# Kernel tuning notes

Measured on AMD Instinct MI355X. Metric: run time of the kernel, lower is better.

Reference implementation:

```python
import jax, jax.numpy as jnp
import numpy as np

N = 50000      # nodes
E = 800000     # edges
IN = 128       # in_channels
HID = 64       # hidden_channels per head
HEADS = 2
OUT = 64       # out_channels of second conv
ED = 16        # edge_dim
NEG = 0.2      # LeakyReLU negative slope (PyG default)


def setup_inputs() -> dict:
    key = jax.random.key(0)
    ks = jax.random.split(key, 24)
    def p(k, shape, scale=0.05):
        return jax.random.normal(k, shape, jnp.float32) * scale
    inp = {}
    inp["x"] = jax.random.normal(ks[0], (N, IN), jnp.float32)
    inp["edge_index"] = jax.random.randint(ks[1], (2, E), 0, N, jnp.int32)
    inp["edge_attr"] = jax.random.normal(ks[2], (E, ED), jnp.float32)
    # GATv2Conv layer 1 (heads=HEADS, out=HID)
    inp["Wl1"] = p(ks[3], (IN, HEADS * HID)); inp["bl1"] = jnp.zeros((HEADS * HID,), jnp.float32)
    inp["Wr1"] = p(ks[4], (IN, HEADS * HID)); inp["br1"] = jnp.zeros((HEADS * HID,), jnp.float32)
    inp["We1"] = p(ks[5], (ED, HEADS * HID))
    inp["att1"] = p(ks[6], (HEADS, HID))
    inp["b1"] = jnp.zeros((HEADS * HID,), jnp.float32)
    # GATv2Conv layer 2 (heads=1, out=OUT), input dim = HEADS*HID
    inp["Wl2"] = p(ks[7], (HEADS * HID, OUT)); inp["bl2"] = jnp.zeros((OUT,), jnp.float32)
    inp["Wr2"] = p(ks[8], (HEADS * HID, OUT)); inp["br2"] = jnp.zeros((OUT,), jnp.float32)
    inp["We2"] = p(ks[9], (ED, OUT))
    inp["att2"] = p(ks[10], (1, OUT))
    inp["b2"] = jnp.zeros((OUT,), jnp.float32)
    # edge MLP: Linear(2*OUT, OUT) -> ReLU -> Linear(OUT, 1)
    inp["Wm1"] = p(ks[11], (2 * OUT, OUT)); inp["bm1"] = jnp.zeros((OUT,), jnp.float32)
    inp["Wm2"] = p(ks[12], (OUT, 1)); inp["bm2"] = jnp.zeros((1,), jnp.float32)
    return inp


def add_self_loops(src, dst, edge_attr, n):
    # PyG add_self_loops with fill_value='mean': loop attr = mean of incoming edge attrs
    cnt = jax.ops.segment_sum(jnp.ones((src.shape[0],), edge_attr.dtype), dst, num_segments=n)
    loop_attr = jax.ops.segment_sum(edge_attr, dst, num_segments=n) / jnp.maximum(cnt, 1.0)[:, None]
    ar = jnp.arange(n, dtype=src.dtype)
    return (jnp.concatenate([src, ar]), jnp.concatenate([dst, ar]),
            jnp.concatenate([edge_attr, loop_attr], axis=0))


def gatv2_layer(x, src, dst, edge_attr, Wl, bl, Wr, br, We, att, bias, heads, out_ch):
    n = x.shape[0]
    xl = (x @ Wl + bl).reshape(n, heads, out_ch)   # messages (source side)
    xr = (x @ Wr + br).reshape(n, heads, out_ch)   # target side
    ea = (edge_attr @ We).reshape(-1, heads, out_ch)
    m = jax.nn.leaky_relu(xl[src] + xr[dst] + ea, NEG)      # [Et, H, C]
    logits = jnp.einsum('ehc,hc->eh', m, att)               # [Et, H]
    # segment softmax over destination node (every node has a self loop)
    mx = jax.ops.segment_max(logits, dst, num_segments=n)
    ex = jnp.exp(logits - mx[dst])
    den = jax.ops.segment_sum(ex, dst, num_segments=n)
    alpha = ex / den[dst]                                   # [Et, H]
    out = jax.ops.segment_sum(alpha[:, :, None] * xl[src], dst, num_segments=n)
    return out.reshape(n, heads * out_ch) + bias


def reference(x, edge_index, edge_attr,
              Wl1, bl1, Wr1, br1, We1, att1, b1,
              Wl2, bl2, Wr2, br2, We2, att2, b2,
              Wm1, bm1, Wm2, bm2):
    src, dst = edge_index[0], edge_index[1]
    n = x.shape[0]
    s2, d2, ea2 = add_self_loops(src, dst, edge_attr, n)
    h = gatv2_layer(x, s2, d2, ea2, Wl1, bl1, Wr1, br1, We1, att1, b1, HEADS, HID)
    h = jax.nn.elu(h)
    h = gatv2_layer(h, s2, d2, ea2, Wl2, bl2, Wr2, br2, We2, att2, b2, 1, OUT)
    # edge predictor over the ORIGINAL edges
    ei = jnp.concatenate([h[src], h[dst]], axis=1)          # [E, 2*OUT]
    z = jax.nn.relu(ei @ Wm1 + bm1)
    return z @ Wm2 + bm2                                    # [E, 1]
```

## Files before the change

kernel.cpp:

```cpp
#include <hip/hip_runtime.h>
#include <cstdint>
#include <cstddef>


__device__ __forceinline__ float half_sum(float v) {
#pragma unroll
  for (int o = 1; o <= 16; o <<= 1) v += __shfl_xor(v, o, 64);
  return v;
}

__global__ __launch_bounds__(256) void cnt_kernel(const int* __restrict__ dst,
                                                  int* __restrict__ cnt, int E) {
  int e = blockIdx.x * 256 + threadIdx.x;
  if (e < E) atomicAdd(&cnt[dst[e]], 1);
}

__global__ __launch_bounds__(1024) void scan_kernel(
    const int* __restrict__ cnt, int* __restrict__ rowptr,
    int* __restrict__ cursor, int Nn) {
  __shared__ int part[1024];
  int t = threadIdx.x;
  int chunk = (Nn + 1023) / 1024;
  int lo = t * chunk, hi = min(lo + chunk, Nn);
  int s = 0;
  for (int i = lo; i < hi; i++) s += cnt[i] + 1;
  part[t] = s;
  __syncthreads();
  for (int o = 1; o < 1024; o <<= 1) {
    int v = (t >= o) ? part[t - o] : 0;
    __syncthreads();
    part[t] += v;
    __syncthreads();
  }
  int run = (t == 0) ? 0 : part[t - 1];
  for (int i = lo; i < hi; i++) {
    rowptr[i] = run;
    cursor[i] = run;
    run += cnt[i] + 1;
  }
  if (t == 1023) rowptr[Nn] = part[1023];
}

__global__ __launch_bounds__(256) void csr_build_kernel(
    const int* __restrict__ src, const int* __restrict__ dst,
    int* __restrict__ cursor, int* __restrict__ eperm,
    int* __restrict__ sperm, int E, int Et) {
  int e = blockIdx.x * 256 + threadIdx.x;
  if (e >= Et) return;
  int s, d;
  if (e < E) { s = src[e]; d = dst[e]; }
  else { s = e - E; d = s; }
  int pos = atomicAdd(&cursor[d], 1);
  eperm[pos] = e;
  sperm[pos] = s;
}

__global__ __launch_bounds__(256) void loop_attr_kernel(
    const int* __restrict__ rowptr, const int* __restrict__ eperm,
    const float* __restrict__ edge_attr, float* __restrict__ loop_attr,
    int Nn, int E) {
  int wid = blockIdx.x * 4 + (threadIdx.x >> 6);
  if (wid >= Nn) return;
  int l = threadIdx.x & 63;
  int sub = l >> 4, kk = l & 15;
  int start = rowptr[wid], end = rowptr[wid + 1];
  float acc = 0.f;
  for (int j = start + sub; j < end; j += 4) {
    int e = eperm[j];
    if (e < E) acc += edge_attr[(size_t)e * 16 + kk];
  }
  acc += __shfl_xor(acc, 16, 64);
  acc += __shfl_xor(acc, 32, 64);
  if (sub == 0) {
    float c = fmaxf((float)(end - start - 1), 1.f);
    loop_attr[(size_t)wid * 16 + kk] = acc / c;
  }
}

template <int K, int NC>
__global__ __launch_bounds__(256) void gemm_kernel(
    const float* __restrict__ A, const float* __restrict__ W,
    const float* __restrict__ bias, float* __restrict__ C, int M) {
  const int BM = 64;
  const int CQ = NC / 4;
  const int RP = BM / (256 / CQ);
  __shared__ float Alds[BM * K];
  int row0 = blockIdx.x * BM;
  for (int i = threadIdx.x; i < BM * K / 4; i += 256) {
    int r = i / (K / 4);
    float4 v = make_float4(0.f, 0.f, 0.f, 0.f);
    if (row0 + r < M) v = ((const float4*)A)[(size_t)(row0 + r) * (K / 4) + (i % (K / 4))];
    ((float4*)Alds)[i] = v;
  }
  __syncthreads();
  int cq = threadIdx.x % CQ;
  int rg = threadIdx.x / CQ;
  float4 acc[RP];
#pragma unroll
  for (int r = 0; r < RP; r++) acc[r] = make_float4(0.f, 0.f, 0.f, 0.f);
  const float4* W4 = (const float4*)W;
  for (int k = 0; k < K; k += 4) {
    float4 w0 = W4[(size_t)(k + 0) * CQ + cq];
    float4 w1 = W4[(size_t)(k + 1) * CQ + cq];
    float4 w2 = W4[(size_t)(k + 2) * CQ + cq];
    float4 w3 = W4[(size_t)(k + 3) * CQ + cq];
#pragma unroll
    for (int r = 0; r < RP; r++) {
      float4 a = ((const float4*)Alds)[(rg * RP + r) * (K / 4) + (k >> 2)];
      acc[r].x = fmaf(a.x, w0.x, acc[r].x);
      acc[r].y = fmaf(a.x, w0.y, acc[r].y);
      acc[r].z = fmaf(a.x, w0.z, acc[r].z);
      acc[r].w = fmaf(a.x, w0.w, acc[r].w);
      acc[r].x = fmaf(a.y, w1.x, acc[r].x);
      acc[r].y = fmaf(a.y, w1.y, acc[r].y);
      acc[r].z = fmaf(a.y, w1.z, acc[r].z);
      acc[r].w = fmaf(a.y, w1.w, acc[r].w);
      acc[r].x = fmaf(a.z, w2.x, acc[r].x);
      acc[r].y = fmaf(a.z, w2.y, acc[r].y);
      acc[r].z = fmaf(a.z, w2.z, acc[r].z);
      acc[r].w = fmaf(a.z, w2.w, acc[r].w);
      acc[r].x = fmaf(a.w, w3.x, acc[r].x);
      acc[r].y = fmaf(a.w, w3.y, acc[r].y);
      acc[r].z = fmaf(a.w, w3.z, acc[r].z);
      acc[r].w = fmaf(a.w, w3.w, acc[r].w);
    }
  }
  float4 b4 = bias ? ((const float4*)bias)[cq] : make_float4(0.f, 0.f, 0.f, 0.f);
#pragma unroll
  for (int r = 0; r < RP; r++) {
    int row = row0 + rg * RP + r;
    if (row < M) {
      float4 o = make_float4(acc[r].x + b4.x, acc[r].y + b4.y,
                             acc[r].z + b4.z, acc[r].w + b4.w);
      ((float4*)C)[(size_t)row * CQ + cq] = o;
    }
  }
}

template <int ELU>
__global__ __launch_bounds__(256) void node_fused2_kernel(
    const int* __restrict__ rowptr, const int* __restrict__ eperm,
    const int* __restrict__ sperm, const float* __restrict__ edge_attr,
    const float* __restrict__ loop_attr, const float* __restrict__ We,
    const float* __restrict__ att, const float* __restrict__ xl,
    const float* __restrict__ xr, const float* __restrict__ bias,
    float* __restrict__ out, int Nn, int E) {
  int wid = blockIdx.x * 4 + (threadIdx.x >> 6);
  if (wid >= Nn) return;
  int l = threadIdx.x & 63;
  int ch = ((l >> 5) << 6) | ((l & 31) << 1);
  float2 we[16];
#pragma unroll
  for (int k = 0; k < 16; k++) we[k] = *(const float2*)(We + k * 128 + ch);
  float2 xr2 = *(const float2*)(xr + (size_t)wid * 128 + ch);
  float2 at2 = *(const float2*)(att + ch);
  int start = __builtin_amdgcn_readfirstlane(rowptr[wid]);
  int end = __builtin_amdgcn_readfirstlane(rowptr[wid + 1]);
  float4 A0, A1, A2, A3;
  float2 X;
  int e_n, s_n;
  {
    int e_c = eperm[start], s_c = sperm[start];
    const float4* p4 = (const float4*)((e_c < E)
                           ? edge_attr + (size_t)e_c * 16
                           : loop_attr + (size_t)(e_c - E) * 16);
    A0 = p4[0]; A1 = p4[1]; A2 = p4[2]; A3 = p4[3];
    X = *(const float2*)(xl + (size_t)s_c * 128 + ch);
    int j1 = min(start + 1, end - 1);
    e_n = eperm[j1];
    s_n = sperm[j1];
  }
  float m = -1e30f, sden = 0.f, accx = 0.f, accy = 0.f;
  for (int j = start; j < end; ++j) {
    int j2 = min(j + 2, end - 1);
    int e2 = eperm[j2], s2 = sperm[j2];
    const float4* p4 = (const float4*)((e_n < E)
                           ? edge_attr + (size_t)e_n * 16
                           : loop_attr + (size_t)(e_n - E) * 16);
    float4 B0 = p4[0], B1 = p4[1], B2 = p4[2], B3 = p4[3];
    float2 Y = *(const float2*)(xl + (size_t)s_n * 128 + ch);
    float av[16] = {A0.x, A0.y, A0.z, A0.w, A1.x, A1.y, A1.z, A1.w,
                    A2.x, A2.y, A2.z, A2.w, A3.x, A3.y, A3.z, A3.w};
    float ex = 0.f, ey = 0.f;
#pragma unroll
    for (int k = 0; k < 16; k++) {
      ex = fmaf(av[k], we[k].x, ex);
      ey = fmaf(av[k], we[k].y, ey);
    }
    float mx = X.x + xr2.x + ex;
    float my = X.y + xr2.y + ey;
    mx = (mx >= 0.f) ? mx : 0.2f * mx;
    my = (my >= 0.f) ? my : 0.2f * my;
    float p = half_sum(fmaf(at2.x, mx, at2.y * my));
    float nm = fmaxf(m, p);
    float r = __expf(m - nm), ep = __expf(p - nm);
    sden = fmaf(sden, r, ep);
    accx = fmaf(accx, r, ep * X.x);
    accy = fmaf(accy, r, ep * X.y);
    m = nm;
    A0 = B0; A1 = B1; A2 = B2; A3 = B3; X = Y;
    e_n = e2; s_n = s2;
  }
  float inv = 1.f / sden;
  float2 b2 = *(const float2*)(bias + ch);
  float vx = fmaf(accx, inv, b2.x);
  float vy = fmaf(accy, inv, b2.y);
  if (ELU) {
    vx = (vx > 0.f) ? vx : expm1f(vx);
    vy = (vy > 0.f) ? vy : expm1f(vy);
  }
  *(float2*)(out + (size_t)wid * 128 + ch) = make_float2(vx, vy);
}

__global__ __launch_bounds__(256) void node_fused1_kernel(
    const int* __restrict__ rowptr, const int* __restrict__ eperm,
    const int* __restrict__ sperm, const float* __restrict__ edge_attr,
    const float* __restrict__ loop_attr, const float* __restrict__ We,
    const float* __restrict__ att, const float* __restrict__ xl,
    const float* __restrict__ xr, const float* __restrict__ bias,
    float* __restrict__ out, int Nn, int E) {
  int wid = blockIdx.x * 4 + (threadIdx.x >> 6);
  if (wid >= Nn) return;
  int l = threadIdx.x & 63;
  int half = l >> 5;
  int ch = (l & 31) << 1;
  float2 we[16];
#pragma unroll
  for (int k = 0; k < 16; k++) we[k] = *(const float2*)(We + k * 64 + ch);
  float2 xr2 = *(const float2*)(xr + (size_t)wid * 64 + ch);
  float2 at2 = *(const float2*)(att + ch);
  int start = __builtin_amdgcn_readfirstlane(rowptr[wid]);
  int end = __builtin_amdgcn_readfirstlane(rowptr[wid + 1]);
  float4 A0, A1, A2, A3;
  float2 X;
  int e_n, s_n;
  {
    int jc = min(start + half, end - 1);
    int e_c = eperm[jc], s_c = sperm[jc];
    const float4* p4 = (const float4*)((e_c < E)
                           ? edge_attr + (size_t)e_c * 16
                           : loop_attr + (size_t)(e_c - E) * 16);
    A0 = p4[0]; A1 = p4[1]; A2 = p4[2]; A3 = p4[3];
    X = *(const float2*)(xl + (size_t)s_c * 64 + ch);
    int j1 = min(start + 2 + half, end - 1);
    e_n = eperm[j1];
    s_n = sperm[j1];
  }
  float m = -1e30f, sden = 0.f, accx = 0.f, accy = 0.f;
  for (int j = start; j < end; j += 2) {
    int j2 = min(j + 4 + half, end - 1);
    int e2 = eperm[j2], s2 = sperm[j2];
    const float4* p4 = (const float4*)((e_n < E)
                           ? edge_attr + (size_t)e_n * 16
                           : loop_attr + (size_t)(e_n - E) * 16);
    float4 B0 = p4[0], B1 = p4[1], B2 = p4[2], B3 = p4[3];
    float2 Y = *(const float2*)(xl + (size_t)s_n * 64 + ch);
    float av[16] = {A0.x, A0.y, A0.z, A0.w, A1.x, A1.y, A1.z, A1.w,
                    A2.x, A2.y, A2.z, A2.w, A3.x, A3.y, A3.z, A3.w};
    float ex = 0.f, ey = 0.f;
#pragma unroll
    for (int k = 0; k < 16; k++) {
      ex = fmaf(av[k], we[k].x, ex);
      ey = fmaf(av[k], we[k].y, ey);
    }
    float mx = X.x + xr2.x + ex;
    float my = X.y + xr2.y + ey;
    mx = (mx >= 0.f) ? mx : 0.2f * mx;
    my = (my >= 0.f) ? my : 0.2f * my;
    float p = half_sum(fmaf(at2.x, mx, at2.y * my));
    bool dead = (j + half) >= end;
    p = dead ? -1e30f : p;
    float nm = fmaxf(m, p);
    float r = __expf(m - nm), ep = __expf(p - nm);
    ep = dead ? 0.f : ep;
    sden = fmaf(sden, r, ep);
    accx = fmaf(accx, r, ep * X.x);
    accy = fmaf(accy, r, ep * X.y);
    m = nm;
    A0 = B0; A1 = B1; A2 = B2; A3 = B3; X = Y;
    e_n = e2; s_n = s2;
  }
  float mo = __shfl_xor(m, 32, 64);
  float so = __shfl_xor(sden, 32, 64);
  float aox = __shfl_xor(accx, 32, 64);
  float aoy = __shfl_xor(accy, 32, 64);
  float M = fmaxf(m, mo);
  float ra = __expf(m - M), rb = __expf(mo - M);
  float S = fmaf(sden, ra, so * rb);
  float AX = fmaf(accx, ra, aox * rb);
  float AY = fmaf(accy, ra, aoy * rb);
  float inv = 1.f / S;
  if (half == 0) {
    float2 b2 = *(const float2*)(bias + ch);
    *(float2*)(out + (size_t)wid * 64 + ch) =
        make_float2(fmaf(AX, inv, b2.x), fmaf(AY, inv, b2.y));
  }
}

__global__ __launch_bounds__(256) void edge_mlp_kernel(
    const int* __restrict__ src, const int* __restrict__ dst,
    const float* __restrict__ aa, const float* __restrict__ bb,
    const float* __restrict__ Wm2, const float* __restrict__ bm2,
    float* __restrict__ out, int E) {
  int t = blockIdx.x * 256 + threadIdx.x;
  int eid = t >> 4;
  if (eid >= E) return;
  int g = threadIdx.x & 15;
  float4 w = ((const float4*)Wm2)[g];
  int s = src[eid], d = dst[eid];
  float4 za = ((const float4*)aa)[(size_t)s * 16 + g];
  float4 zb = ((const float4*)bb)[(size_t)d * 16 + g];
  float p = fmaxf(za.x + zb.x, 0.f) * w.x;
  p = fmaf(fmaxf(za.y + zb.y, 0.f), w.y, p);
  p = fmaf(fmaxf(za.z + zb.z, 0.f), w.z, p);
  p = fmaf(fmaxf(za.w + zb.w, 0.f), w.w, p);
#pragma unroll
  for (int o = 8; o > 0; o >>= 1) p += __shfl_xor(p, o, 64);
  if (g == 0) out[eid] = p + bm2[0];
}

extern "C" void kernel_launch(void* const* d_in, const int* in_sizes, int n_in,
                              void* d_out, int out_size, void* d_ws,
                              size_t ws_size, hipStream_t stream) {
  const float* x = (const float*)d_in[0];
  const int* ei = (const int*)d_in[1];
  const float* edge_attr = (const float*)d_in[2];
  const float* Wl1 = (const float*)d_in[3];
  const float* bl1 = (const float*)d_in[4];
  const float* Wr1 = (const float*)d_in[5];
  const float* br1 = (const float*)d_in[6];
  const float* We1 = (const float*)d_in[7];
  const float* att1 = (const float*)d_in[8];
  const float* b1 = (const float*)d_in[9];
  const float* Wl2 = (const float*)d_in[10];
  const float* bl2 = (const float*)d_in[11];
  const float* Wr2 = (const float*)d_in[12];
  const float* br2 = (const float*)d_in[13];
  const float* We2 = (const float*)d_in[14];
  const float* att2 = (const float*)d_in[15];
  const float* b2 = (const float*)d_in[16];
  const float* Wm1 = (const float*)d_in[17];
  const float* bm1 = (const float*)d_in[18];
  const float* Wm2 = (const float*)d_in[19];
  const float* bm2 = (const float*)d_in[20];

  const int Nn = in_sizes[0] / 128;
  const int E = in_sizes[1] / 2;
  const int Et = E + Nn;
  const int* src = ei;
  const int* dst = ei + E;

  char* ws = (char*)d_ws;
  size_t off = 0;
  auto alloc = [&](size_t bytes) -> char* {
    char* p = ws + off;
    off += (bytes + 255) & ~(size_t)255;
    return p;
  };
  int* cnt = (int*)alloc((size_t)Nn * 4);
  float* loop_attr = (float*)alloc((size_t)Nn * 16 * 4);
  int* rowptr = (int*)alloc((size_t)(Nn + 1) * 4);
  int* cursor = (int*)alloc((size_t)Nn * 4);
  int* eperm = (int*)alloc((size_t)Et * 4);
  int* sperm = (int*)alloc((size_t)Et * 4);
  float* xl = (float*)alloc((size_t)Nn * 128 * 4);
  float* xr = (float*)alloc((size_t)Nn * 128 * 4);
  float* h1 = (float*)alloc((size_t)Nn * 128 * 4);
  float* h2 = (float*)alloc((size_t)Nn * 64 * 4);
  float* aa = xl;
  float* bb = xr;

  hipMemsetAsync(cnt, 0, (size_t)Nn * 4, stream);

  cnt_kernel<<<(E + 255) / 256, 256, 0, stream>>>(dst, cnt, E);
  scan_kernel<<<1, 1024, 0, stream>>>(cnt, rowptr, cursor, Nn);
  csr_build_kernel<<<(Et + 255) / 256, 256, 0, stream>>>(src, dst, cursor, eperm,
                                                         sperm, E, Et);
  loop_attr_kernel<<<(Nn + 3) / 4, 256, 0, stream>>>(rowptr, eperm, edge_attr,
                                                     loop_attr, Nn, E);

  gemm_kernel<128, 128><<<(Nn + 63) / 64, 256, 0, stream>>>(x, Wl1, bl1, xl, Nn);
  gemm_kernel<128, 128><<<(Nn + 63) / 64, 256, 0, stream>>>(x, Wr1, br1, xr, Nn);
  node_fused2_kernel<1><<<(Nn + 3) / 4, 256, 0, stream>>>(
      rowptr, eperm, sperm, edge_attr, loop_attr, We1, att1, xl, xr, b1, h1, Nn, E);

  gemm_kernel<128, 64><<<(Nn + 63) / 64, 256, 0, stream>>>(h1, Wl2, bl2, xl, Nn);
  gemm_kernel<128, 64><<<(Nn + 63) / 64, 256, 0, stream>>>(h1, Wr2, br2, xr, Nn);
  node_fused1_kernel<<<(Nn + 3) / 4, 256, 0, stream>>>(
      rowptr, eperm, sperm, edge_attr, loop_attr, We2, att2, xl, xr, b2, h2, Nn, E);

  gemm_kernel<64, 64><<<(Nn + 63) / 64, 256, 0, stream>>>(h2, Wm1, nullptr, aa, Nn);
  gemm_kernel<64, 64><<<(Nn + 63) / 64, 256, 0, stream>>>(h2, Wm1 + 64 * 64, bm1,
                                                          bb, Nn);
  edge_mlp_kernel<<<(E * 16 + 255) / 256, 256, 0, stream>>>(src, dst, aa, bb,
                                                            Wm2, bm2,
                                                            (float*)d_out, E);
}
```

Before: 798.0 us.

## Fold self-loop edges into node kernels, fuse paired GEMMs, parallelize CSR scan

Self-loops are no longer stored in the CSR. Each node kernel handles its own loop edge at the end, taking the loop edge projection as the mean of the incoming edge projections accumulated in the loop. By linearity this equals projecting the mean attribute, so the separate loop_attr kernel and the per-edge branch go away. The eperm/sperm arrays are merged into one int2 array, and the single-block serial scan is replaced by a three-kernel parallel scan. Paired GEMMs sharing an input are fused into one kernel that reads A once and writes two outputs, at the cost of higher register pressure under a launch-bounds occupancy hint.

```diff
diff --git a/kernel.cpp b/kernel.cpp
--- a/kernel.cpp
+++ b/kernel.cpp
@@ -15,72 +15,73 @@
   if (e < E) atomicAdd(&cnt[dst[e]], 1);
 }
 
-__global__ __launch_bounds__(1024) void scan_kernel(
-    const int* __restrict__ cnt, int* __restrict__ rowptr,
-    int* __restrict__ cursor, int Nn) {
-  __shared__ int part[1024];
+__global__ __launch_bounds__(256) void scan_blocksum_kernel(
+    const int* __restrict__ cnt, int* __restrict__ partial, int Nn) {
+  int i = blockIdx.x * 256 + threadIdx.x;
+  int v = (i < Nn) ? cnt[i] : 0;
+#pragma unroll
+  for (int o = 32; o > 0; o >>= 1) v += __shfl_xor(v, o, 64);
+  __shared__ int ws[4];
+  if ((threadIdx.x & 63) == 0) ws[threadIdx.x >> 6] = v;
+  __syncthreads();
+  if (threadIdx.x == 0) partial[blockIdx.x] = ws[0] + ws[1] + ws[2] + ws[3];
+}
+
+__global__ __launch_bounds__(256) void scan_partial_kernel(
+    int* __restrict__ partial, int* __restrict__ rowptr, int nb, int Nn, int E) {
+  __shared__ int buf[256];
   int t = threadIdx.x;
-  int chunk = (Nn + 1023) / 1024;
-  int lo = t * chunk, hi = min(lo + chunk, Nn);
-  int s = 0;
-  for (int i = lo; i < hi; i++) s += cnt[i] + 1;
-  part[t] = s;
+  int v = (t < nb) ? partial[t] : 0;
+  buf[t] = v;
   __syncthreads();
-  for (int o = 1; o < 1024; o <<= 1) {
-    int v = (t >= o) ? part[t - o] : 0;
+  for (int o = 1; o < 256; o <<= 1) {
+    int u = (t >= o) ? buf[t - o] : 0;
     __syncthreads();
-    part[t] += v;
+    buf[t] += u;
     __syncthreads();
   }
-  int run = (t == 0) ? 0 : part[t - 1];
-  for (int i = lo; i < hi; i++) {
-    rowptr[i] = run;
-    cursor[i] = run;
-    run += cnt[i] + 1;
-  }
-  if (t == 1023) rowptr[Nn] = part[1023];
+  partial[t] = (t == 0) ? 0 : buf[t - 1];
+  if (t == 0) rowptr[Nn] = E;
+}
+
+__global__ __launch_bounds__(256) void scan_write_kernel(
+    const int* __restrict__ cnt, const int* __restrict__ partial,
+    int* __restrict__ rowptr, int* __restrict__ cursor, int Nn) {
+  __shared__ int buf[256];
+  int i = blockIdx.x * 256 + threadIdx.x;
+  int t = threadIdx.x;
+  int v = (i < Nn) ? cnt[i] : 0;
+  buf[t] = v;
+  __syncthreads();
+  for (int o = 1; o < 256; o <<= 1) {
+    int u = (t >= o) ? buf[t - o] : 0;
+    __syncthreads();
+    buf[t] += u;
+    __syncthreads();
+  }
+  if (i < Nn) {
+    int r = partial[blockIdx.x] + buf[t] - v;
+    rowptr[i] = r;
+    cursor[i] = r;
+  }
 }
 
 __global__ __launch_bounds__(256) void csr_build_kernel(
     const int* __restrict__ src, const int* __restrict__ dst,
-    int* __restrict__ cursor, int* __restrict__ eperm,
-    int* __restrict__ sperm, int E, int Et) {
+    int* __restrict__ cursor, int2* __restrict__ es, int E) {
   int e = blockIdx.x * 256 + threadIdx.x;
-  if (e >= Et) return;
-  int s, d;
-  if (e < E) { s = src[e]; d = dst[e]; }
-  else { s = e - E; d = s; }
+  if (e >= E) return;
+  int s = src[e], d = dst[e];
   int pos = atomicAdd(&cursor[d], 1);
-  eperm[pos] = e;
-  sperm[pos] = s;
-}
-
-__global__ __launch_bounds__(256) void loop_attr_kernel(
-    const int* __restrict__ rowptr, const int* __restrict__ eperm,
-    const float* __restrict__ edge_attr, float* __restrict__ loop_attr,
-    int Nn, int E) {
-  int wid = blockIdx.x * 4 + (threadIdx.x >> 6);
-  if (wid >= Nn) return;
-  int l = threadIdx.x & 63;
-  int sub = l >> 4, kk = l & 15;
-  int start = rowptr[wid], end = rowptr[wid + 1];
-  float acc = 0.f;
-  for (int j = start + sub; j < end; j += 4) {
-    int e = eperm[j];
-    if (e < E) acc += edge_attr[(size_t)e * 16 + kk];
-  }
-  acc += __shfl_xor(acc, 16, 64);
-  acc += __shfl_xor(acc, 32, 64);
-  if (sub == 0) {
-    float c = fmaxf((float)(end - start - 1), 1.f);
-    loop_attr[(size_t)wid * 16 + kk] = acc / c;
-  }
+  es[pos] = make_int2(e, s);
 }
 
 template <int K, int NC>
-__global__ __launch_bounds__(256) void gemm_kernel(
-    const float* __restrict__ A, const float* __restrict__ W,
-    const float* __restrict__ bias, float* __restrict__ C, int M) {
+__global__ __launch_bounds__(256, 4) void gemm2_kernel(
+    const float* __restrict__ A, const float* __restrict__ W1,
+    const float* __restrict__ b1, float* __restrict__ C1,
+    const float* __restrict__ W2, const float* __restrict__ b2,
+    float* __restrict__ C2, int M) {
   const int BM = 64;
   const int CQ = NC / 4;
   const int RP = BM / (256 / CQ);
@@ -95,56 +96,83 @@
   __syncthreads();
   int cq = threadIdx.x % CQ;
   int rg = threadIdx.x / CQ;
-  float4 acc[RP];
-#pragma unroll
-  for (int r = 0; r < RP; r++) acc[r] = make_float4(0.f, 0.f, 0.f, 0.f);
-  const float4* W4 = (const float4*)W;
+  float4 acc1[RP], acc2[RP];
+#pragma unroll
+  for (int r = 0; r < RP; r++) {
+    acc1[r] = make_float4(0.f, 0.f, 0.f, 0.f);
+    acc2[r] = make_float4(0.f, 0.f, 0.f, 0.f);
+  }
+  const float4* W14 = (const float4*)W1;
+  const float4* W24 = (const float4*)W2;
   for (int k = 0; k < K; k += 4) {
-    float4 w0 = W4[(size_t)(k + 0) * CQ + cq];
-    float4 w1 = W4[(size_t)(k + 1) * CQ + cq];
-    float4 w2 = W4[(size_t)(k + 2) * CQ + cq];
-    float4 w3 = W4[(size_t)(k + 3) * CQ + cq];
+    float4 u0 = W14[(size_t)(k + 0) * CQ + cq];
+    float4 u1 = W14[(size_t)(k + 1) * CQ + cq];
+    float4 u2 = W14[(size_t)(k + 2) * CQ + cq];
+    float4 u3 = W14[(size_t)(k + 3) * CQ + cq];
+    float4 v0 = W24[(size_t)(k + 0) * CQ + cq];
+    float4 v1 = W24[(size_t)(k + 1) * CQ + cq];
+    float4 v2 = W24[(size_t)(k + 2) * CQ + cq];
+    float4 v3 = W24[(size_t)(k + 3) * CQ + cq];
 #pragma unroll
     for (int r = 0; r < RP; r++) {
       float4 a = ((const float4*)Alds)[(rg * RP + r) * (K / 4) + (k >> 2)];
-      acc[r].x = fmaf(a.x, w0.x, acc[r].x);
-      acc[r].y = fmaf(a.x, w0.y, acc[r].y);
-      acc[r].z = fmaf(a.x, w0.z, acc[r].z);
-      acc[r].w = fmaf(a.x, w0.w, acc[r].w);
-      acc[r].x = fmaf(a.y, w1.x, acc[r].x);
-      acc[r].y = fmaf(a.y, w1.y, acc[r].y);
-      acc[r].z = fmaf(a.y, w1.z, acc[r].z);
-      acc[r].w = fmaf(a.y, w1.w, acc[r].w);
-      acc[r].x = fmaf(a.z, w2.x, acc[r].x);
-      acc[r].y = fmaf(a.z, w2.y, acc[r].y);
-      acc[r].z = fmaf(a.z, w2.z, acc[r].z);
-      acc[r].w = fmaf(a.z, w2.w, acc[r].w);
-      acc[r].x = fmaf(a.w, w3.x, acc[r].x);
-      acc[r].y = fmaf(a.w, w3.y, acc[r].y);
-      acc[r].z = fmaf(a.w, w3.z, acc[r].z);
-      acc[r].w = fmaf(a.w, w3.w, acc[r].w);
-    }
-  }
-  float4 b4 = bias ? ((const float4*)bias)[cq] : make_float4(0.f, 0.f, 0.f, 0.f);
+      acc1[r].x = fmaf(a.x, u0.x, acc1[r].x);
+      acc1[r].y = fmaf(a.x, u0.y, acc1[r].y);
+      acc1[r].z = fmaf(a.x, u0.z, acc1[r].z);
+      acc1[r].w = fmaf(a.x, u0.w, acc1[r].w);
+      acc1[r].x = fmaf(a.y, u1.x, acc1[r].x);
+      acc1[r].y = fmaf(a.y, u1.y, acc1[r].y);
+      acc1[r].z = fmaf(a.y, u1.z, acc1[r].z);
+      acc1[r].w = fmaf(a.y, u1.w, acc1[r].w);
+      acc1[r].x = fmaf(a.z, u2.x, acc1[r].x);
+      acc1[r].y = fmaf(a.z, u2.y, acc1[r].y);
+      acc1[r].z = fmaf(a.z, u2.z, acc1[r].z);
+      acc1[r].w = fmaf(a.z, u2.w, acc1[r].w);
+      acc1[r].x = fmaf(a.w, u3.x, acc1[r].x);
+      acc1[r].y = fmaf(a.w, u3.y, acc1[r].y);
+      acc1[r].z = fmaf(a.w, u3.z, acc1[r].z);
+      acc1[r].w = fmaf(a.w, u3.w, acc1[r].w);
+      acc2[r].x = fmaf(a.x, v0.x, acc2[r].x);
+      acc2[r].y = fmaf(a.x, v0.y, acc2[r].y);
+      acc2[r].z = fmaf(a.x, v0.z, acc2[r].z);
+      acc2[r].w = fmaf(a.x, v0.w, acc2[r].w);
+      acc2[r].x = fmaf(a.y, v1.x, acc2[r].x);
+      acc2[r].y = fmaf(a.y, v1.y, acc2[r].y);
+      acc2[r].z = fmaf(a.y, v1.z, acc2[r].z);
+      acc2[r].w = fmaf(a.y, v1.w, acc2[r].w);
+      acc2[r].x = fmaf(a.z, v2.x, acc2[r].x);
+      acc2[r].y = fmaf(a.z, v2.y, acc2[r].y);
+      acc2[r].z = fmaf(a.z, v2.z, acc2[r].z);
+      acc2[r].w = fmaf(a.z, v2.w, acc2[r].w);
+      acc2[r].x = fmaf(a.w, v3.x, acc2[r].x);
+      acc2[r].y = fmaf(a.w, v3.y, acc2[r].y);
+      acc2[r].z = fmaf(a.w, v3.z, acc2[r].z);
+      acc2[r].w = fmaf(a.w, v3.w, acc2[r].w);
+    }
+  }
+  float4 bb1 = b1 ? ((const float4*)b1)[cq] : make_float4(0.f, 0.f, 0.f, 0.f);
+  float4 bb2 = b2 ? ((const float4*)b2)[cq] : make_float4(0.f, 0.f, 0.f, 0.f);
 #pragma unroll
   for (int r = 0; r < RP; r++) {
     int row = row0 + rg * RP + r;
     if (row < M) {
-      float4 o = make_float4(acc[r].x + b4.x, acc[r].y + b4.y,
-                             acc[r].z + b4.z, acc[r].w + b4.w);
-      ((float4*)C)[(size_t)row * CQ + cq] = o;
+      ((float4*)C1)[(size_t)row * CQ + cq] =
+          make_float4(acc1[r].x + bb1.x, acc1[r].y + bb1.y, acc1[r].z + bb1.z,
+                      acc1[r].w + bb1.w);
+      ((float4*)C2)[(size_t)row * CQ + cq] =
+          make_float4(acc2[r].x + bb2.x, acc2[r].y + bb2.y, acc2[r].z + bb2.z,
+                      acc2[r].w + bb2.w);
     }
   }
 }
 
 template <int ELU>
-__global__ __launch_bounds__(256) void node_fused2_kernel(
-    const int* __restrict__ rowptr, const int* __restrict__ eperm,
-    const int* __restrict__ sperm, const float* __restrict__ edge_attr,
-    const float* __restrict__ loop_attr, const float* __restrict__ We,
+__global__ __launch_bounds__(256, 4) void node_fused2_kernel(
+    const int* __restrict__ rowptr, const int2* __restrict__ es,
+    const float* __restrict__ edge_attr, const float* __restrict__ We,
     const float* __restrict__ att, const float* __restrict__ xl,
     const float* __restrict__ xr, const float* __restrict__ bias,
-    float* __restrict__ out, int Nn, int E) {
+    float* __restrict__ out, int Nn) {
   int wid = blockIdx.x * 4 + (threadIdx.x >> 6);
   if (wid >= Nn) return;
   int l = threadIdx.x & 63;
@@ -156,50 +184,62 @@
   float2 at2 = *(const float2*)(att + ch);
   int start = __builtin_amdgcn_readfirstlane(rowptr[wid]);
   int end = __builtin_amdgcn_readfirstlane(rowptr[wid + 1]);
-  float4 A0, A1, A2, A3;
-  float2 X;
-  int e_n, s_n;
+  float m = -1e30f, sden = 0.f, accx = 0.f, accy = 0.f;
+  float sax = 0.f, say = 0.f;
+  if (end > start) {
+    float4 A0, A1, A2, A3;
+    float2 X;
+    int2 en;
+    {
+      int2 ec = es[start];
+      const float4* p4 = (const float4*)(edge_attr + (size_t)ec.x * 16);
+      A0 = p4[0]; A1 = p4[1]; A2 = p4[2]; A3 = p4[3];
+      X = *(const float2*)(xl + (size_t)ec.y * 128 + ch);
+      en = es[min(start + 1, end - 1)];
+    }
+    for (int j = start; j < end; ++j) {
+      int2 e2 = es[min(j + 2, end - 1)];
+      const float4* p4 = (const float4*)(edge_attr + (size_t)en.x * 16);
+      float4 B0 = p4[0], B1 = p4[1], B2 = p4[2], B3 = p4[3];
+      float2 Y = *(const float2*)(xl + (size_t)en.y * 128 + ch);
+      float av[16] = {A0.x, A0.y, A0.z, A0.w, A1.x, A1.y, A1.z, A1.w,
+                      A2.x, A2.y, A2.z, A2.w, A3.x, A3.y, A3.z, A3.w};
+      float ex = 0.f, ey = 0.f;
+#pragma unroll
+      for (int k = 0; k < 16; k++) {
+        ex = fmaf(av[k], we[k].x, ex);
+        ey = fmaf(av[k], we[k].y, ey);
+      }
+      sax += ex;
+      say += ey;
+      float mx = X.x + xr2.x + ex;
+      float my = X.y + xr2.y + ey;
+      mx = (mx >= 0.f) ? mx : 0.2f * mx;
+      my = (my >= 0.f) ? my : 0.2f * my;
+      float p = half_sum(fmaf(at2.x, mx, at2.y * my));
+      float nm = fmaxf(m, p);
+      float r = __expf(m - nm), ep = __expf(p - nm);
+      sden = fmaf(sden, r, ep);
+      accx = fmaf(accx, r, ep * X.x);
+      accy = fmaf(accy, r, ep * X.y);
+      m = nm;
+      A0 = B0; A1 = B1; A2 = B2; A3 = B3; X = Y;
+      en = e2;
+    }
+  }
   {
-    int e_c = eperm[start], s_c = sperm[start];
-    const float4* p4 = (const float4*)((e_c < E)
-                           ? edge_attr + (size_t)e_c * 16
-                           : loop_attr + (size_t)(e_c - E) * 16);
-    A0 = p4[0]; A1 = p4[1]; A2 = p4[2]; A3 = p4[3];
-    X = *(const float2*)(xl + (size_t)s_c * 128 + ch);
-    int j1 = min(start + 1, end - 1);
-    e_n = eperm[j1];
-    s_n = sperm[j1];
-  }
-  float m = -1e30f, sden = 0.f, accx = 0.f, accy = 0.f;
-  for (int j = start; j < end; ++j) {
-    int j2 = min(j + 2, end - 1);
-    int e2 = eperm[j2], s2 = sperm[j2];
-    const float4* p4 = (const float4*)((e_n < E)
-                           ? edge_attr + (size_t)e_n * 16
-                           : loop_attr + (size_t)(e_n - E) * 16);
-    float4 B0 = p4[0], B1 = p4[1], B2 = p4[2], B3 = p4[3];
-    float2 Y = *(const float2*)(xl + (size_t)s_n * 128 + ch);
-    float av[16] = {A0.x, A0.y, A0.z, A0.w, A1.x, A1.y, A1.z, A1.w,
-                    A2.x, A2.y, A2.z, A2.w, A3.x, A3.y, A3.z, A3.w};
-    float ex = 0.f, ey = 0.f;
-#pragma unroll
-    for (int k = 0; k < 16; k++) {
-      ex = fmaf(av[k], we[k].x, ex);
-      ey = fmaf(av[k], we[k].y, ey);
-    }
-    float mx = X.x + xr2.x + ex;
-    float my = X.y + xr2.y + ey;
+    float denom = 1.f / fmaxf((float)(end - start), 1.f);
+    float2 Xs = *(const float2*)(xl + (size_t)wid * 128 + ch);
+    float mx = Xs.x + xr2.x + sax * denom;
+    float my = Xs.y + xr2.y + say * denom;
     mx = (mx >= 0.f) ? mx : 0.2f * mx;
     my = (my >= 0.f) ? my : 0.2f * my;
     float p = half_sum(fmaf(at2.x, mx, at2.y * my));
     float nm = fmaxf(m, p);
     float r = __expf(m - nm), ep = __expf(p - nm);
     sden = fmaf(sden, r, ep);
-    accx = fmaf(accx, r, ep * X.x);
-    accy = fmaf(accy, r, ep * X.y);
-    m = nm;
-    A0 = B0; A1 = B1; A2 = B2; A3 = B3; X = Y;
-    e_n = e2; s_n = s2;
+    accx = fmaf(accx, r, ep * Xs.x);
+    accy = fmaf(accy, r, ep * Xs.y);
   }
   float inv = 1.f / sden;
   float2 b2 = *(const float2*)(bias + ch);
@@ -212,13 +252,12 @@
   *(float2*)(out + (size_t)wid * 128 + ch) = make_float2(vx, vy);
 }
 
-__global__ __launch_bounds__(256) void node_fused1_kernel(
-    const int* __restrict__ rowptr, const int* __restrict__ eperm,
-    const int* __restrict__ sperm, const float* __restrict__ edge_attr,
-    const float* __restrict__ loop_attr, const float* __restrict__ We,
+__global__ __launch_bounds__(256, 4) void node_fused1_kernel(
+    const int* __restrict__ rowptr, const int2* __restrict__ es,
+    const float* __restrict__ edge_attr, const float* __restrict__ We,
     const float* __restrict__ att, const float* __restrict__ xl,
     const float* __restrict__ xr, const float* __restrict__ bias,
-    float* __restrict__ out, int Nn, int E) {
+    float* __restrict__ out, int Nn) {
   int wid = blockIdx.x * 4 + (threadIdx.x >> 6);
   if (wid >= Nn) return;
   int l = threadIdx.x & 63;
@@ -231,54 +270,52 @@
   float2 at2 = *(const float2*)(att + ch);
   int start = __builtin_amdgcn_readfirstlane(rowptr[wid]);
   int end = __builtin_amdgcn_readfirstlane(rowptr[wid + 1]);
-  float4 A0, A1, A2, A3;
-  float2 X;
-  int e_n, s_n;
-  {
-    int jc = min(start + half, end - 1);
-    int e_c = eperm[jc], s_c = sperm[jc];
-    const float4* p4 = (const float4*)((e_c < E)
-                           ? edge_attr + (size_t)e_c * 16
-                           : loop_attr + (size_t)(e_c - E) * 16);
-    A0 = p4[0]; A1 = p4[1]; A2 = p4[2]; A3 = p4[3];
-    X = *(const float2*)(xl + (size_t)s_c * 64 + ch);
-    int j1 = min(start + 2 + half, end - 1);
-    e_n = eperm[j1];
-    s_n = sperm[j1];
-  }
   float m = -1e30f, sden = 0.f, accx = 0.f, accy = 0.f;
-  for (int j = start; j < end; j += 2) {
-    int j2 = min(j + 4 + half, end - 1);
-    int e2 = eperm[j2], s2 = sperm[j2];
-    const float4* p4 = (const float4*)((e_n < E)
-                           ? edge_attr + (size_t)e_n * 16
-                           : loop_attr + (size_t)(e_n - E) * 16);
-    float4 B0 = p4[0], B1 = p4[1], B2 = p4[2], B3 = p4[3];
-    float2 Y = *(const float2*)(xl + (size_t)s_n * 64 + ch);
-    float av[16] = {A0.x, A0.y, A0.z, A0.w, A1.x, A1.y, A1.z, A1.w,
-                    A2.x, A2.y, A2.z, A2.w, A3.x, A3.y, A3.z, A3.w};
-    float ex = 0.f, ey = 0.f;
-#pragma unroll
-    for (int k = 0; k < 16; k++) {
-      ex = fmaf(av[k], we[k].x, ex);
-      ey = fmaf(av[k], we[k].y, ey);
-    }
-    float mx = X.x + xr2.x + ex;
-    float my = X.y + xr2.y + ey;
-    mx = (mx >= 0.f) ? mx : 0.2f * mx;
-    my = (my >= 0.f) ? my : 0.2f * my;
-    float p = half_sum(fmaf(at2.x, mx, at2.y * my));
-    bool dead = (j + half) >= end;
-    p = dead ? -1e30f : p;
-    float nm = fmaxf(m, p);
-    float r = __expf(m - nm), ep = __expf(p - nm);
-    ep = dead ? 0.f : ep;
-    sden = fmaf(sden, r, ep);
-    accx = fmaf(accx, r, ep * X.x);
-    accy = fmaf(accy, r, ep * X.y);
-    m = nm;
-    A0 = B0; A1 = B1; A2 = B2; A3 = B3; X = Y;
-    e_n = e2; s_n = s2;
+  float sax = 0.f, say = 0.f;
+  if (end > start) {
+    float4 A0, A1, A2, A3;
+    float2 X;
+    int2 en;
+    {
+      int jc = min(start + half, end - 1);
+      int2 ec = es[jc];
+      const float4* p4 = (const float4*)(edge_attr + (size_t)ec.x * 16);
+      A0 = p4[0]; A1 = p4[1]; A2 = p4[2]; A3 = p4[3];
+      X = *(const float2*)(xl + (size_t)ec.y * 64 + ch);
+      en = es[min(start + 2 + half, end - 1)];
+    }
+    for (int j = start; j < end; j += 2) {
+      int2 e2 = es[min(j + 4 + half, end - 1)];
+      const float4* p4 = (const float4*)(edge_attr + (size_t)en.x * 16);
+      float4 B0 = p4[0], B1 = p4[1], B2 = p4[2], B3 = p4[3];
+      float2 Y = *(const float2*)(xl + (size_t)en.y * 64 + ch);
+      float av[16] = {A0.x, A0.y, A0.z, A0.w, A1.x, A1.y, A1.z, A1.w,
+                      A2.x, A2.y, A2.z, A2.w, A3.x, A3.y, A3.z, A3.w};
+      float ex = 0.f, ey = 0.f;
+#pragma unroll
+      for (int k = 0; k < 16; k++) {
+        ex = fmaf(av[k], we[k].x, ex);
+        ey = fmaf(av[k], we[k].y, ey);
+      }
+      bool dead = (j + half) >= end;
+      sax += dead ? 0.f : ex;
+      say += dead ? 0.f : ey;
+      float mx = X.x + xr2.x + ex;
+      float my = X.y + xr2.y + ey;
+      mx = (mx >= 0.f) ? mx : 0.2f * mx;
+      my = (my >= 0.f) ? my : 0.2f * my;
+      float p = half_sum(fmaf(at2.x, mx, at2.y * my));
+      p = dead ? -1e30f : p;
+      float nm = fmaxf(m, p);
+      float r = __expf(m - nm), ep = __expf(p - nm);
+      ep = dead ? 0.f : ep;
+      sden = fmaf(sden, r, ep);
+      accx = fmaf(accx, r, ep * X.x);
+      accy = fmaf(accy, r, ep * X.y);
+      m = nm;
+      A0 = B0; A1 = B1; A2 = B2; A3 = B3; X = Y;
+      en = e2;
+    }
   }
   float mo = __shfl_xor(m, 32, 64);
   float so = __shfl_xor(sden, 32, 64);
@@ -289,8 +326,24 @@
   float S = fmaf(sden, ra, so * rb);
   float AX = fmaf(accx, ra, aox * rb);
   float AY = fmaf(accy, ra, aoy * rb);
-  float inv = 1.f / S;
+  float saxt = sax + __shfl_xor(sax, 32, 64);
+  float sayt = say + __shfl_xor(say, 32, 64);
+  {
+    float denom = 1.f / fmaxf((float)(end - start), 1.f);
+    float2 Xs = *(const float2*)(xl + (size_t)wid * 64 + ch);
+    float mx = Xs.x + xr2.x + saxt * denom;
+    float my = Xs.y + xr2.y + sayt * denom;
+    mx = (mx >= 0.f) ? mx : 0.2f * mx;
+    my = (my >= 0.f) ? my : 0.2f * my;
+    float p = half_sum(fmaf(at2.x, mx, at2.y * my));
+    float nm = fmaxf(M, p);
+    float r = __expf(M - nm), ep = __expf(p - nm);
+    S = fmaf(S, r, ep);
+    AX = fmaf(AX, r, ep * Xs.x);
+    AY = fmaf(AY, r, ep * Xs.y);
+  }
   if (half == 0) {
+    float inv = 1.f / S;
     float2 b2 = *(const float2*)(bias + ch);
     *(float2*)(out + (size_t)wid * 64 + ch) =
         make_float2(fmaf(AX, inv, b2.x), fmaf(AY, inv, b2.y));
@@ -346,9 +399,9 @@
 
   const int Nn = in_sizes[0] / 128;
   const int E = in_sizes[1] / 2;
-  const int Et = E + Nn;
   const int* src = ei;
   const int* dst = ei + E;
+  const int nb = (Nn + 255) / 256;
 
   char* ws = (char*)d_ws;
   size_t off = 0;
@@ -358,11 +411,10 @@
     return p;
   };
   int* cnt = (int*)alloc((size_t)Nn * 4);
-  float* loop_attr = (float*)alloc((size_t)Nn * 16 * 4);
   int* rowptr = (int*)alloc((size_t)(Nn + 1) * 4);
   int* cursor = (int*)alloc((size_t)Nn * 4);
-  int* eperm = (int*)alloc((size_t)Et * 4);
-  int* sperm = (int*)alloc((size_t)Et * 4);
+  int* partial = (int*)alloc(256 * 4);
+  int2* es = (int2*)alloc((size_t)E * 8);
   float* xl = (float*)alloc((size_t)Nn * 128 * 4);
   float* xr = (float*)alloc((size_t)Nn * 128 * 4);
   float* h1 = (float*)alloc((size_t)Nn * 128 * 4);
@@ -373,25 +425,23 @@
   hipMemsetAsync(cnt, 0, (size_t)Nn * 4, stream);
 
   cnt_kernel<<<(E + 255) / 256, 256, 0, stream>>>(dst, cnt, E);
-  scan_kernel<<<1, 1024, 0, stream>>>(cnt, rowptr, cursor, Nn);
-  csr_build_kernel<<<(Et + 255) / 256, 256, 0, stream>>>(src, dst, cursor, eperm,
-                                                         sperm, E, Et);
-  loop_attr_kernel<<<(Nn + 3) / 4, 256, 0, stream>>>(rowptr, eperm, edge_attr,
-                                                     loop_attr, Nn, E);
-
-  gemm_kernel<128, 128><<<(Nn + 63) / 64, 256, 0, stream>>>(x, Wl1, bl1, xl, Nn);
-  gemm_kernel<128, 128><<<(Nn + 63) / 64, 256, 0, stream>>>(x, Wr1, br1, xr, Nn);
+  scan_blocksum_kernel<<<nb, 256, 0, stream>>>(cnt, partial, Nn);
+  scan_partial_kernel<<<1, 256, 0, stream>>>(partial, rowptr, nb, Nn, E);
+  scan_write_kernel<<<nb, 256, 0, stream>>>(cnt, partial, rowptr, cursor, Nn);
+  csr_build_kernel<<<(E + 255) / 256, 256, 0, stream>>>(src, dst, cursor, es, E);
+
+  gemm2_kernel<128, 128><<<(Nn + 63) / 64, 256, 0, stream>>>(
+      x, Wl1, bl1, xl, Wr1, br1, xr, Nn);
   node_fused2_kernel<1><<<(Nn + 3) / 4, 256, 0, stream>>>(
-      rowptr, eperm, sperm, edge_attr, loop_attr, We1, att1, xl, xr, b1, h1, Nn, E);
-
-  gemm_kernel<128, 64><<<(Nn + 63) / 64, 256, 0, stream>>>(h1, Wl2, bl2, xl, Nn);
-  gemm_kernel<128, 64><<<(Nn + 63) / 64, 256, 0, stream>>>(h1, Wr2, br2, xr, Nn);
+      rowptr, es, edge_attr, We1, att1, xl, xr, b1, h1, Nn);
+
+  gemm2_kernel<128, 64><<<(Nn + 63) / 64, 256, 0, stream>>>(
+      h1, Wl2, bl2, xl, Wr2, br2, xr, Nn);
   node_fused1_kernel<<<(Nn + 3) / 4, 256, 0, stream>>>(
-      rowptr, eperm, sperm, edge_attr, loop_attr, We2, att2, xl, xr, b2, h2, Nn, E);
-
-  gemm_kernel<64, 64><<<(Nn + 63) / 64, 256, 0, stream>>>(h2, Wm1, nullptr, aa, Nn);
-  gemm_kernel<64, 64><<<(Nn + 63) / 64, 256, 0, stream>>>(h2, Wm1 + 64 * 64, bm1,
-                                                          bb, Nn);
+      rowptr, es, edge_attr, We2, att2, xl, xr, b2, h2, Nn);
+
+  gemm2_kernel<64, 64><<<(Nn + 63) / 64, 256, 0, stream>>>(
+      h2, Wm1, nullptr, aa, Wm1 + 64 * 64, bm1, bb, Nn);
   edge_mlp_kernel<<<(E * 16 + 255) / 256, 256, 0, stream>>>(src, dst, aa, bb,
                                                             Wm2, bm2,
                                                             (float*)d_out, E);
```

Result: faster. 676.8 us (-15.2%).
